# Optimization experiments

Measured on AMD Instinct MI355X. Metric: run time of the kernel, lower is better.

## Reference

```python
import jax, jax.numpy as jnp
import numpy as np

B, N, F_IN = 4, 2048, 256
K, D = 4, 64
NEG_SLOPE = 0.2


def setup_inputs() -> dict:
    key = jax.random.key(0)
    k1, k2, k3, k4, k5 = jax.random.split(key, 5)
    x = jax.random.normal(k1, (B, N, F_IN), dtype=jnp.float32)
    adj = jax.random.randint(k2, (B, N, N), 0, 2, dtype=jnp.int32)
    # xavier_uniform-style params
    def xavier(k, shape):
        fan_in, fan_out = shape[-2], shape[-1]
        lim = np.sqrt(6.0 / (fan_in + fan_out))
        return jax.random.uniform(k, shape, jnp.float32, -lim, lim)
    W = xavier(k3, (K, F_IN, D))
    a_src = xavier(k4, (K, D, 1))
    a_dst = xavier(k5, (K, D, 1))
    return {"x": x, "adj": adj, "W": W, "a_src": a_src, "a_dst": a_dst}


def reference(x, adj, W, a_src, a_dst):
    # Wh: (B, K, N, D)
    Wh = jnp.einsum('bnf,kfd->bknd', x, W)
    e_src = jnp.einsum('bknd,kdo->bkno', Wh, a_src)  # (B,K,N,1)
    e_dst = jnp.einsum('bknd,kdo->bkno', Wh, a_dst)  # (B,K,N,1)
    e = e_src + jnp.swapaxes(e_dst, -2, -1)          # (B,K,N,N)
    e = jnp.where(e > 0, e, NEG_SLOPE * e)           # LeakyReLU(0.2)
    # adjacency mask with forced self-loops (adj + I > 0)
    eye = jnp.eye(e.shape[-1], dtype=bool)
    mask = (adj[:, None, :, :] > 0) | eye            # (B,1|K,N,N)
    e = jnp.where(mask, e, -jnp.inf)
    # numerically-stable softmax matching F_module_softmax
    x_max = jnp.max(e, axis=-1, keepdims=True)
    x_max = jnp.where(jnp.isinf(x_max), 0.0, x_max)
    exp_e = jnp.exp(e - x_max)
    exp_e = jnp.where(jnp.isinf(e), 0.0, exp_e)
    alpha = exp_e / (jnp.sum(exp_e, axis=-1, keepdims=True) + 1e-10)
    # dropout is identity in eval mode
    out = jnp.matmul(alpha, Wh)                      # (B,K,N,D)
    # concat heads: (B,N,K*D)
    Bn, Kn, Nn, Dn = out.shape
    return jnp.transpose(out, (0, 2, 1, 3)).reshape(Bn, Nn, Kn * Dn)
```

## Files before the change

### kernel.cpp

```cpp
#include <hip/hip_runtime.h>

#define NB 4
#define NN 2048
#define NF 256
#define NK 4
#define ND 64
#define NEG 0.2f
#define LOG2E 1.4426950408889634f

typedef _Float16 f16;
typedef _Float16 f16x2 __attribute__((ext_vector_type(2)));
typedef _Float16 f16x4 __attribute__((ext_vector_type(4)));
typedef _Float16 f16x8 __attribute__((ext_vector_type(8)));
typedef float f32x4 __attribute__((ext_vector_type(4)));
typedef float f32x16 __attribute__((ext_vector_type(16)));
typedef unsigned int u32;
typedef unsigned short u16;

__global__ __launch_bounds__(256) void k01(
    const float* __restrict__ x,
    const int*   __restrict__ adj,
    const float* __restrict__ Wm,
    const float* __restrict__ a_src,
    const float* __restrict__ a_dst,
    unsigned int* __restrict__ abit,
    f16* __restrict__ wht,
    float* __restrict__ sbuf,
    f16* __restrict__ ebuf,
    f16* __restrict__ fbuf)
{
    __shared__ f16 wt[64 * 256];

    const int bx  = blockIdx.x;
    const int tid = threadIdx.x;

    if (bx >= 256) {
        const int row = (bx - 256) * 4 + (tid >> 6);
        const int l   = tid & 63;
        const int i   = row & (NN - 1);
        const int* __restrict__ ar = adj + (size_t)row * NN;

        int v[32];
#pragma unroll
        for (int c = 0; c < 32; ++c) v[c] = ar[c * 64 + l];

        unsigned int kx = 0, ky = 0;
#pragma unroll
        for (int c = 0; c < 32; ++c) {
            unsigned long long m = __ballot(v[c] > 0);
            if (l == c) { kx = (unsigned int)m; ky = (unsigned int)(m >> 32); }
        }
        if (l == (i >> 6)) {
            unsigned int sb = 1u << (i & 31);
            if (((i >> 5) & 1) == 0) kx |= sb; else ky |= sb;
        }
        if (l < 32) {
            uint2 kk; kk.x = kx; kk.y = ky;
            *(uint2*)&abit[(size_t)row * 64 + l * 2] = kk;
        }
        return;
    }

    const int gx  = bx & 15;
    const int k   = (bx >> 4) & 3;
    const int b   = bx >> 6;
    const int wv  = tid >> 6;
    const int l   = tid & 63;
    const int q   = l >> 4;
    const int r16 = l & 15;

#pragma unroll
    for (int p = 0; p < 16; ++p) {
        const int f  = p * 16 + (tid >> 4);
        const int d0 = (tid & 15) * 4;
        float4 wv4 = *(const float4*)&Wm[(size_t)(k * NF + f) * ND + d0];
        wt[(d0 + 0) * 256 + (f ^ (((d0 + 0) & 7) << 3))] = (f16)wv4.x;
        wt[(d0 + 1) * 256 + (f ^ (((d0 + 1) & 7) << 3))] = (f16)wv4.y;
        wt[(d0 + 2) * 256 + (f ^ (((d0 + 2) & 7) << 3))] = (f16)wv4.z;
        wt[(d0 + 3) * 256 + (f ^ (((d0 + 3) & 7) << 3))] = (f16)wv4.w;
    }
    __syncthreads();

    const int ncol0 = gx * 128 + wv * 32;
    f32x4 acc[2][4];
#pragma unroll
    for (int nt = 0; nt < 2; ++nt)
#pragma unroll
        for (int dt = 0; dt < 4; ++dt)
            acc[nt][dt] = (f32x4){0.f, 0.f, 0.f, 0.f};

    for (int fs = 0; fs < 16; ++fs) {
        const int f0 = fs * 16 + q * 4;
        f16x4 af[4];
#pragma unroll
        for (int dt = 0; dt < 4; ++dt) {
            int d = dt * 16 + r16;
            af[dt] = *(const f16x4*)&wt[d * 256 + (f0 ^ ((d & 7) << 3))];
        }
#pragma unroll
        for (int nt = 0; nt < 2; ++nt) {
            int n = ncol0 + nt * 16 + r16;
            float4 xv = *(const float4*)&x[((size_t)(b * NN + n)) * NF + f0];
            f16x4 bf = {(f16)xv.x, (f16)xv.y, (f16)xv.z, (f16)xv.w};
#pragma unroll
            for (int dt = 0; dt < 4; ++dt)
                acc[nt][dt] = __builtin_amdgcn_mfma_f32_16x16x16f16(
                    af[dt], bf, acc[nt][dt], 0, 0, 0);
        }
    }

    float asv[4][4], adv[4][4];
#pragma unroll
    for (int dt = 0; dt < 4; ++dt)
#pragma unroll
        for (int rr = 0; rr < 4; ++rr) {
            int d = dt * 16 + q * 4 + rr;
            asv[dt][rr] = a_src[k * ND + d];
            adv[dt][rr] = a_dst[k * ND + d];
        }

#pragma unroll
    for (int nt = 0; nt < 2; ++nt) {
        int n = ncol0 + nt * 16 + r16;
        float sp = 0.f, tp = 0.f;
#pragma unroll
        for (int dt = 0; dt < 4; ++dt)
#pragma unroll
            for (int rr = 0; rr < 4; ++rr) {
                sp += acc[nt][dt][rr] * asv[dt][rr];
                tp += acc[nt][dt][rr] * adv[dt][rr];
            }
        sp += __shfl_xor(sp, 16);
        sp += __shfl_xor(sp, 32);
        tp += __shfl_xor(tp, 16);
        tp += __shfl_xor(tp, 32);
        if (q == 0) {
            int idx = (b * NK + k) * NN + n;
            sbuf[idx] = sp;
            ebuf[idx] = (f16)__builtin_exp2f(tp * LOG2E);
            fbuf[idx] = (f16)__builtin_exp2f(0.2f * LOG2E * tp);
        }
    }

    __syncthreads();
    f16* lt = wt;
#pragma unroll
    for (int nt = 0; nt < 2; ++nt) {
        const int nl = wv * 32 + nt * 16 + r16;
#pragma unroll
        for (int dt = 0; dt < 4; ++dt)
#pragma unroll
            for (int rr = 0; rr < 4; ++rr) {
                int d = dt * 16 + q * 4 + rr;
                lt[d * 136 + nl] = (f16)acc[nt][dt][rr];
            }
    }
    __syncthreads();
    {
        const size_t obase = (size_t)(b * NK + k) * 131072 + (size_t)gx * 8192;
        const int o  = tid >> 4;
        const int d0 = (tid & 15) * 4;
#pragma unroll
        for (int z = 0; z < 4; ++z) {
            f16x8 v8 = *(const f16x8*)&lt[(d0 + z) * 136 + o * 8];
            *(f16x8*)&wht[obase + (size_t)o * 512 + (d0 + z) * 8] = v8;
        }
    }
}

__global__ __launch_bounds__(512) void k2_attn(
    const unsigned int* __restrict__ abit,
    const f16* __restrict__ wht,
    const float* __restrict__ sbuf,
    const f16* __restrict__ ebuf,
    const f16* __restrict__ fbuf,
    float* __restrict__ out)
{
    const int bid = blockIdx.x;
    const int bkv = (bid & 7) | (((bid >> 3) & 1) << 3);
    const int rg  = bid >> 4;
    const int b   = bkv >> 2, k = bkv & 3;
    const int i0  = rg * 64;
    const int tid = threadIdx.x;
    const int w   = tid >> 6;
    const int l   = tid & 63;
    const int r32 = l & 31;
    const int hi  = l >> 5;
    const int row_a = i0 + r32;
    const int row_b = i0 + 32 + r32;

    __shared__ __attribute__((aligned(16))) char pool[75776];
    u16*   el      = (u16*)(pool + 65536);
    u16*   fl      = (u16*)(pool + 69632);
    float* ddenbuf = (float*)(pool + 73728);

    {
        const u16* eb = (const u16*)(ebuf + bkv * NN);
        const u16* fb = (const u16*)(fbuf + bkv * NN);
        *(uint2*)&el[tid * 4] = *(const uint2*)&eb[tid * 4];
        *(uint2*)&fl[tid * 4] = *(const uint2*)&fb[tid * 4];
    }

    const float s_a = sbuf[bkv * NN + row_a];
    const float s_b = sbuf[bkv * NN + row_b];
    const f16 Afa = (f16)__builtin_exp2f(0.8f * LOG2E * fminf(s_a, 0.f));
    const f16 Bfa = (f16)__builtin_exp2f(-0.8f * LOG2E * fmaxf(s_a, 0.f));
    const f16 Afb = (f16)__builtin_exp2f(0.8f * LOG2E * fminf(s_b, 0.f));
    const f16 Bfb = (f16)__builtin_exp2f(-0.8f * LOG2E * fmaxf(s_b, 0.f));
    const f16x2 Af2a = {Afa, Afa}, Bf2a = {Bfa, Bfa};
    const f16x2 Af2b = {Afb, Afb}, Bf2b = {Bfb, Bfb};
    const f16x2 one2 = {(f16)1.0f, (f16)1.0f};

    const unsigned int* __restrict__ abrow_a =
        abit + (size_t)(b * NN + row_a) * 64 + w * 8;
    const unsigned int* __restrict__ abrow_b = abrow_a + 32 * 64;
    uint2 abx_a[4], abx_b[4];
#pragma unroll
    for (int it = 0; it < 4; ++it) {
        abx_a[it] = *(const uint2*)(abrow_a + it * 2);
        abx_b[it] = *(const uint2*)(abrow_b + it * 2);
    }

    const f16* __restrict__ lanep =
        wht + (size_t)bkv * 131072 + (size_t)(w * 32 + hi) * 512 + r32 * 8;

    float den_a = 0.f, den_b = 0.f;
    f32x16 acc[4];
#pragma unroll
    for (int t = 0; t < 4; ++t)
#pragma unroll
        for (int z = 0; z < 16; ++z) acc[t][z] = 0.f;

    __syncthreads();

#define PABUILD(PA, DEN, AF2, BF2, WORD)                                       \
    do {                                                                       \
        const u32 bbyte = ((WORD) >> (((jts & 1) << 4) + (hi << 3))) & 0xffu;  \
        const u32 u = (bbyte << 15) | bbyte;                                   \
        u32 pa_u[4];                                                           \
        _Pragma("unroll") for (int p = 0; p < 4; ++p) {                        \
            f16x2 e2 = __builtin_bit_cast(f16x2, ((const u32*)&E4)[p]);        \
            f16x2 f2 = __builtin_bit_cast(f16x2, ((const u32*)&F4)[p]);        \
            f16x2 w2 = __builtin_elementwise_max((AF2) * e2, (BF2) * f2);      \
            u32 xx = (u >> (2 * p)) & 0x00010001u;                             \
            u32 mm = (xx << 16) - xx;                                          \
            pa_u[p] = __builtin_bit_cast(u32, w2) & mm;                        \
            DEN = __builtin_amdgcn_fdot2(                                      \
                __builtin_bit_cast(f16x2, pa_u[p]), one2, DEN, false);         \
        }                                                                      \
        uint4 pav = {pa_u[0], pa_u[1], pa_u[2], pa_u[3]};                      \
        PA = __builtin_bit_cast(f16x8, pav);                                   \
    } while (0)

#define FRAG_ADDR(st) (lanep + (size_t)(((st) >> 2) * 8 + ((st) & 3) * 2) * 512)
#define JB(st) (w * 256 + ((st) >> 2) * 64 + ((st) & 3) * 16 + hi * 8)

    f16x8 vf[3][2];
    uint4 EF[2][2];
    vf[0][0] = *(const f16x8*)(FRAG_ADDR(0));
    vf[0][1] = *(const f16x8*)(FRAG_ADDR(0) + 256);
    vf[1][0] = *(const f16x8*)(FRAG_ADDR(1));
    vf[1][1] = *(const f16x8*)(FRAG_ADDR(1) + 256);
    EF[0][0] = *(const uint4*)&el[JB(0)];
    EF[0][1] = *(const uint4*)&fl[JB(0)];

#pragma unroll
    for (int st = 0; st < 16; ++st) {
        const int it = st >> 2, jts = st & 3;
        if (st < 14) {
            vf[(st + 2) % 3][0] = *(const f16x8*)(FRAG_ADDR(st + 2));
            vf[(st + 2) % 3][1] = *(const f16x8*)(FRAG_ADDR(st + 2) + 256);
        }
        if (st < 15) {
            EF[(st + 1) & 1][0] = *(const uint4*)&el[JB(st + 1)];
            EF[(st + 1) & 1][1] = *(const uint4*)&fl[JB(st + 1)];
        }
        const uint4 E4 = EF[st & 1][0];
        const uint4 F4 = EF[st & 1][1];
        const u32 word_a = (jts & 2) ? abx_a[it].y : abx_a[it].x;
        const u32 word_b = (jts & 2) ? abx_b[it].y : abx_b[it].x;
        f16x8 pa_a, pa_b;
        PABUILD(pa_a, den_a, Af2a, Bf2a, word_a);
        PABUILD(pa_b, den_b, Af2b, Bf2b, word_b);

        const f16x8 v80 = vf[st % 3][0];
        const f16x8 v81 = vf[st % 3][1];
        acc[0] = __builtin_amdgcn_mfma_f32_32x32x16_f16(pa_a, v80, acc[0], 0, 0, 0);
        acc[1] = __builtin_amdgcn_mfma_f32_32x32x16_f16(pa_a, v81, acc[1], 0, 0, 0);
        acc[2] = __builtin_amdgcn_mfma_f32_32x32x16_f16(pa_b, v80, acc[2], 0, 0, 0);
        acc[3] = __builtin_amdgcn_mfma_f32_32x32x16_f16(pa_b, v81, acc[3], 0, 0, 0);
    }
#undef PABUILD
#undef FRAG_ADDR
#undef JB

    den_a += __shfl_xor(den_a, 32);
    den_b += __shfl_xor(den_b, 32);
    if (hi == 0) {
        ddenbuf[w * 64 + r32]      = den_a;
        ddenbuf[w * 64 + 32 + r32] = den_b;
    }

#define TDUMP(reg)                                                             \
    do {                                                                       \
        float* rb = (float*)(pool + (reg) * 16384) + l * 64;                   \
        _Pragma("unroll") for (int t = 0; t < 4; ++t)                          \
        _Pragma("unroll") for (int sub = 0; sub < 4; ++sub) {                  \
            f32x4 vv = {acc[t][sub * 4], acc[t][sub * 4 + 1],                  \
                        acc[t][sub * 4 + 2], acc[t][sub * 4 + 3]};             \
            *(f32x4*)&rb[((t * 4 + sub) ^ (l & 15)) << 2] = vv;                \
        }                                                                      \
    } while (0)
#define TADD(reg)                                                              \
    do {                                                                       \
        const float* rb = (const float*)(pool + (reg) * 16384) + l * 64;       \
        _Pragma("unroll") for (int t = 0; t < 4; ++t)                          \
        _Pragma("unroll") for (int sub = 0; sub < 4; ++sub) {                  \
            f32x4 vv = *(const f32x4*)&rb[((t * 4 + sub) ^ (l & 15)) << 2];    \
            _Pragma("unroll") for (int m = 0; m < 4; ++m)                      \
                acc[t][sub * 4 + m] += vv[m];                                  \
        }                                                                      \
    } while (0)

    __syncthreads();
    if (w >= 4) TDUMP(w - 4);
    __syncthreads();
    if (w < 4) TADD(w);
    if (w == 2 || w == 3) TDUMP(w);
    __syncthreads();
    if (w < 2) TADD(w + 2);
    if (w == 1) TDUMP(1);
    __syncthreads();
    if (w == 0) {
        TADD(1);
        float* dsum = (float*)(pool + 16384);
        float dd = 0.f;
#pragma unroll
        for (int ww = 0; ww < 8; ++ww) dd += ddenbuf[ww * 64 + l];
        dsum[l] = 1.f / (dd + 1e-10f);
        float* op = out + ((size_t)(b * NN) + i0) * (NK * ND) + k * ND;
#pragma unroll
        for (int t = 0; t < 4; ++t)
#pragma unroll
            for (int rr = 0; rr < 16; ++rr) {
                const int row = (t >> 1) * 32 + (rr & 3) + 8 * (rr >> 2) + 4 * hi;
                op[(size_t)row * (NK * ND) + (t & 1) * 32 + r32] =
                    acc[t][rr] * dsum[row];
            }
    }
#undef TDUMP
#undef TADD
}

extern "C" void kernel_launch(void* const* d_in, const int* in_sizes, int n_in,
                              void* d_out, int out_size, void* d_ws, size_t ws_size,
                              hipStream_t stream) {
    const float* x     = (const float*)d_in[0];
    const int*   adj   = (const int*)d_in[1];
    const float* Wm    = (const float*)d_in[2];
    const float* a_src = (const float*)d_in[3];
    const float* a_dst = (const float*)d_in[4];
    float* out = (float*)d_out;

    char* ws = (char*)d_ws;
    f16*   wht  = (f16*)ws;
    float* sbuf = (float*)(ws + (4u << 20));
    f16*   ebuf = (f16*)(ws + (4u << 20) + (128u << 10));
    f16*   fbuf = (f16*)(ws + (4u << 20) + (192u << 10));
    unsigned int* abit = (unsigned int*)(ws + (4u << 20) + (256u << 10));

    k01<<<dim3(256 + NB * NN / 4), 256, 0, stream>>>(
        x, adj, Wm, a_src, a_dst, abit, wht, sbuf, ebuf, fbuf);
    k2_attn<<<dim3(512), 512, 0, stream>>>(
        abit, wht, sbuf, ebuf, fbuf, out);
}
```

Before: 41.20 us.

## Fuse adjacency bit-packing into attention kernel and regroup heads per XCD

Removes the separate adjacency-to-bitmask pass from the first kernel. The attention kernel now reads int32 adjacency rows directly inside its main loop and patches in the self-loop diagonal. Blocks are remapped so that the four heads sharing a batch and row group land on the same XCD, so the adjacency rows can be reused from L2 or MALL across heads. This saves the bitmask write, the bitmask read-back and the wide second grid of the first kernel. In exchange the attention kernel moves much more adjacency data through the cache, and those loads sit on the loop's critical path without prefetching.

Result: slower. 61.19 us (+48.5%).

```diff
diff --git a/kernel.cpp b/kernel.cpp
--- a/kernel.cpp
+++ b/kernel.cpp
@@ -17,13 +17,11 @@
 typedef unsigned int u32;
 typedef unsigned short u16;
 
-__global__ __launch_bounds__(256) void k01(
+__global__ __launch_bounds__(256) void k1_gemm(
     const float* __restrict__ x,
-    const int*   __restrict__ adj,
     const float* __restrict__ Wm,
     const float* __restrict__ a_src,
     const float* __restrict__ a_dst,
-    unsigned int* __restrict__ abit,
     f16* __restrict__ wht,
     float* __restrict__ sbuf,
     f16* __restrict__ ebuf,
@@ -33,34 +31,6 @@
 
     const int bx  = blockIdx.x;
     const int tid = threadIdx.x;
-
-    if (bx >= 256) {
-        const int row = (bx - 256) * 4 + (tid >> 6);
-        const int l   = tid & 63;
-        const int i   = row & (NN - 1);
-        const int* __restrict__ ar = adj + (size_t)row * NN;
-
-        int v[32];
-#pragma unroll
-        for (int c = 0; c < 32; ++c) v[c] = ar[c * 64 + l];
-
-        unsigned int kx = 0, ky = 0;
-#pragma unroll
-        for (int c = 0; c < 32; ++c) {
-            unsigned long long m = __ballot(v[c] > 0);
-            if (l == c) { kx = (unsigned int)m; ky = (unsigned int)(m >> 32); }
-        }
-        if (l == (i >> 6)) {
-            unsigned int sb = 1u << (i & 31);
-            if (((i >> 5) & 1) == 0) kx |= sb; else ky |= sb;
-        }
-        if (l < 32) {
-            uint2 kk; kk.x = kx; kk.y = ky;
-            *(uint2*)&abit[(size_t)row * 64 + l * 2] = kk;
-        }
-        return;
-    }
-
     const int gx  = bx & 15;
     const int k   = (bx >> 4) & 3;
     const int b   = bx >> 6;
@@ -169,7 +139,7 @@
 }
 
 __global__ __launch_bounds__(512) void k2_attn(
-    const unsigned int* __restrict__ abit,
+    const int* __restrict__ adj,
     const f16* __restrict__ wht,
     const float* __restrict__ sbuf,
     const f16* __restrict__ ebuf,
@@ -177,9 +147,13 @@
     float* __restrict__ out)
 {
     const int bid = blockIdx.x;
-    const int bkv = (bid & 7) | (((bid >> 3) & 1) << 3);
-    const int rg  = bid >> 4;
-    const int b   = bkv >> 2, k = bkv & 3;
+    const int xcd = bid & 7;
+    const int t_  = bid >> 3;
+    const int k   = t_ & 3;
+    const int g   = (t_ >> 2) * 8 + xcd;
+    const int b   = g >> 5;
+    const int rg  = g & 31;
+    const int bkv = b * NK + k;
     const int i0  = rg * 64;
     const int tid = threadIdx.x;
     const int w   = tid >> 6;
@@ -211,15 +185,12 @@
     const f16x2 Af2b = {Afb, Afb}, Bf2b = {Bfb, Bfb};
     const f16x2 one2 = {(f16)1.0f, (f16)1.0f};
 
-    const unsigned int* __restrict__ abrow_a =
-        abit + (size_t)(b * NN + row_a) * 64 + w * 8;
-    const unsigned int* __restrict__ abrow_b = abrow_a + 32 * 64;
-    uint2 abx_a[4], abx_b[4];
-#pragma unroll
-    for (int it = 0; it < 4; ++it) {
-        abx_a[it] = *(const uint2*)(abrow_a + it * 2);
-        abx_b[it] = *(const uint2*)(abrow_b + it * 2);
-    }
+    const int* __restrict__ arow_a = adj + (size_t)(b * NN + row_a) * NN;
+    const int* __restrict__ arow_b = arow_a + (size_t)32 * NN;
+
+    const bool wdiag = (w == (rg >> 2));
+    const int  jda   = row_a - w * 256;
+    const int  jdb   = row_b - w * 256;
 
     const f16* __restrict__ lanep =
         wht + (size_t)bkv * 131072 + (size_t)(w * 32 + hi) * 512 + r32 * 8;
@@ -233,23 +204,32 @@
 
     __syncthreads();
 
-#define PABUILD(PA, DEN, AF2, BF2, WORD)                                       \
+#define PABUILD(PA, DEN, AF2, BF2, V0, V1)                                     \
     do {                                                                       \
-        const u32 bbyte = ((WORD) >> (((jts & 1) << 4) + (hi << 3))) & 0xffu;  \
-        const u32 u = (bbyte << 15) | bbyte;                                   \
+        const int vv[8] = {(V0).x, (V0).y, (V0).z, (V0).w,                     \
+                           (V1).x, (V1).y, (V1).z, (V1).w};                    \
         u32 pa_u[4];                                                           \
         _Pragma("unroll") for (int p = 0; p < 4; ++p) {                        \
             f16x2 e2 = __builtin_bit_cast(f16x2, ((const u32*)&E4)[p]);        \
             f16x2 f2 = __builtin_bit_cast(f16x2, ((const u32*)&F4)[p]);        \
             f16x2 w2 = __builtin_elementwise_max((AF2) * e2, (BF2) * f2);      \
-            u32 xx = (u >> (2 * p)) & 0x00010001u;                             \
-            u32 mm = (xx << 16) - xx;                                          \
+            u32 mm = (vv[2 * p] ? 0x0000FFFFu : 0u) |                          \
+                     (vv[2 * p + 1] ? 0xFFFF0000u : 0u);                       \
             pa_u[p] = __builtin_bit_cast(u32, w2) & mm;                        \
             DEN = __builtin_amdgcn_fdot2(                                      \
                 __builtin_bit_cast(f16x2, pa_u[p]), one2, DEN, false);         \
         }                                                                      \
         uint4 pav = {pa_u[0], pa_u[1], pa_u[2], pa_u[3]};                      \
         PA = __builtin_bit_cast(f16x8, pav);                                   \
+    } while (0)
+
+#define DIAGPATCH(V0, V1, JD, ST)                                              \
+    do {                                                                       \
+        const int jr = (JD) - (ST) * 16 - hi * 8;                              \
+        (V0).x |= (jr == 0); (V0).y |= (jr == 1);                              \
+        (V0).z |= (jr == 2); (V0).w |= (jr == 3);                              \
+        (V1).x |= (jr == 4); (V1).y |= (jr == 5);                              \
+        (V1).z |= (jr == 6); (V1).w |= (jr == 7);                              \
     } while (0)
 
 #define FRAG_ADDR(st) (lanep + (size_t)(((st) >> 2) * 8 + ((st) & 3) * 2) * 512)
@@ -266,7 +246,6 @@
 
 #pragma unroll
     for (int st = 0; st < 16; ++st) {
-        const int it = st >> 2, jts = st & 3;
         if (st < 14) {
             vf[(st + 2) % 3][0] = *(const f16x8*)(FRAG_ADDR(st + 2));
             vf[(st + 2) % 3][1] = *(const f16x8*)(FRAG_ADDR(st + 2) + 256);
@@ -275,13 +254,21 @@
             EF[(st + 1) & 1][0] = *(const uint4*)&el[JB(st + 1)];
             EF[(st + 1) & 1][1] = *(const uint4*)&fl[JB(st + 1)];
         }
+        const int ja = JB(st);
+        int4 va0 = *(const int4*)&arow_a[ja];
+        int4 va1 = *(const int4*)&arow_a[ja + 4];
+        int4 vb0 = *(const int4*)&arow_b[ja];
+        int4 vb1 = *(const int4*)&arow_b[ja + 4];
+        if (wdiag) {
+            DIAGPATCH(va0, va1, jda, st);
+            DIAGPATCH(vb0, vb1, jdb, st);
+        }
+
         const uint4 E4 = EF[st & 1][0];
         const uint4 F4 = EF[st & 1][1];
-        const u32 word_a = (jts & 2) ? abx_a[it].y : abx_a[it].x;
-        const u32 word_b = (jts & 2) ? abx_b[it].y : abx_b[it].x;
         f16x8 pa_a, pa_b;
-        PABUILD(pa_a, den_a, Af2a, Bf2a, word_a);
-        PABUILD(pa_b, den_b, Af2b, Bf2b, word_b);
+        PABUILD(pa_a, den_a, Af2a, Bf2a, va0, va1);
+        PABUILD(pa_b, den_b, Af2b, Bf2b, vb0, vb1);
 
         const f16x8 v80 = vf[st % 3][0];
         const f16x8 v81 = vf[st % 3][1];
@@ -291,6 +278,7 @@
         acc[3] = __builtin_amdgcn_mfma_f32_32x32x16_f16(pa_b, v81, acc[3], 0, 0, 0);
     }
 #undef PABUILD
+#undef DIAGPATCH
 #undef FRAG_ADDR
 #undef JB
 
@@ -367,10 +355,9 @@
     float* sbuf = (float*)(ws + (4u << 20));
     f16*   ebuf = (f16*)(ws + (4u << 20) + (128u << 10));
     f16*   fbuf = (f16*)(ws + (4u << 20) + (192u << 10));
-    unsigned int* abit = (unsigned int*)(ws + (4u << 20) + (256u << 10));
-
-    k01<<<dim3(256 + NB * NN / 4), 256, 0, stream>>>(
-        x, adj, Wm, a_src, a_dst, abit, wht, sbuf, ebuf, fbuf);
+
+    k1_gemm<<<dim3(256), 256, 0, stream>>>(
+        x, Wm, a_src, a_dst, wht, sbuf, ebuf, fbuf);
     k2_attn<<<dim3(512), 512, 0, stream>>>(
-        abit, wht, sbuf, ebuf, fbuf, out);
+        adj, wht, sbuf, ebuf, fbuf, out);
 }
```
